# Kernel tuning notes

Measured on AMD Instinct MI355X. Metric: run time of the kernel, lower is better.

The kernel has to match this reference:

```python
import jax, jax.numpy as jnp
import numpy as np

B, C, H, W, RED = 32, 128, 32, 32, 8
CR = C // RED


def pw(w, x):
    # 1x1 conv as channel contraction: w [O,Cin], x [B,Cin,H,W]
    return jnp.einsum('oc,bchw->bohw', w, x)


def dw(x, k):
    # depthwise 3x3, SAME padding; k [C,1,3,3]
    return jax.lax.conv_general_dilated(
        x, k, (1, 1), 'SAME', feature_group_count=C,
        dimension_numbers=('NCHW', 'OIHW', 'NCHW'))


def setup_inputs() -> dict:
    key = jax.random.key(0)
    ks = jax.random.split(key, 32)
    s = 0.05
    d = {
        'h_t': jax.random.normal(ks[0], (B, C, H, W), jnp.float32),
        'm_prev': jax.random.normal(ks[1], (B, C, H, W), jnp.float32),
        'wq_h': jax.random.normal(ks[2], (CR, C)) * s,
        'wk_h': jax.random.normal(ks[3], (CR, C)) * s,
        'wv_h': jax.random.normal(ks[4], (C, C)) * s,
        'wk_m': jax.random.normal(ks[5], (CR, C)) * s,
        'wv_m': jax.random.normal(ks[6], (C, C)) * s,
        'wz_w': jax.random.normal(ks[7], (C, 2 * C)) * s,
        'wz_b': jnp.zeros((C,)),
        'wmi_dw': jax.random.normal(ks[8], (C, 1, 3, 3)) * s,
        'wmi_pw': jax.random.normal(ks[9], (C, C)) * s,
        'whi_dw': jax.random.normal(ks[10], (C, 1, 3, 3)) * s,
        'whi_pw': jax.random.normal(ks[11], (C, C)) * s,
        'bi': jnp.zeros((C,)),
        'wmg_dw': jax.random.normal(ks[12], (C, 1, 3, 3)) * s,
        'wmg_pw': jax.random.normal(ks[13], (C, C)) * s,
        'whg_dw': jax.random.normal(ks[14], (C, 1, 3, 3)) * s,
        'whg_pw': jax.random.normal(ks[15], (C, C)) * s,
        'bg': jnp.zeros((C,)),
        'wmo_dw': jax.random.normal(ks[16], (C, 1, 3, 3)) * s,
        'wmo_pw': jax.random.normal(ks[17], (C, C)) * s,
        'who_dw': jax.random.normal(ks[18], (C, 1, 3, 3)) * s,
        'who_pw': jax.random.normal(ks[19], (C, C)) * s,
        'bo': jnp.zeros((C,)),
        'wf_w': jax.random.normal(ks[20], (C, C)) * s,
        'wf_b': jnp.zeros((C,)),
    }
    return d


def reference(h_t, m_prev, wq_h, wk_h, wv_h, wk_m, wv_m, wz_w, wz_b,
              wmi_dw, wmi_pw, whi_dw, whi_pw, bi,
              wmg_dw, wmg_pw, whg_dw, whg_pw, bg,
              wmo_dw, wmo_pw, who_dw, who_pw, bo, wf_w, wf_b):
    b, c, h, w = h_t.shape
    N = h * w
    # shared-Q dual attention; Q/K are [B,Cr,N], V are [B,C,N]
    Q = pw(wq_h, h_t).reshape(b, -1, N)
    K_h = pw(wk_h, h_t).reshape(b, -1, N)
    V_h = pw(wv_h, h_t).reshape(b, c, N)
    attn_h = jax.nn.softmax(jnp.einsum('bki,bkj->bij', Q, K_h), axis=-1)  # [B,N,N]
    Z_h = jnp.einsum('bcj,bij->bci', V_h, attn_h).reshape(b, c, h, w)
    K_m = pw(wk_m, m_prev).reshape(b, -1, N)
    V_m = pw(wv_m, m_prev).reshape(b, c, N)
    attn_m = jax.nn.softmax(jnp.einsum('bki,bkj->bij', Q, K_m), axis=-1)
    Z_m = jnp.einsum('bcj,bij->bci', V_m, attn_m).reshape(b, c, h, w)
    Z = pw(wz_w, jnp.concatenate([Z_h, Z_m], axis=1)) + wz_b[None, :, None, None]
    # ConvLSTM-style gated fusion (depthwise 3x3 + pointwise 1x1 pairs)
    i_t = jax.nn.sigmoid(pw(wmi_pw, dw(Z, wmi_dw)) + pw(whi_pw, dw(h_t, whi_dw)) + bi[None, :, None, None])
    g_t = jnp.tanh(pw(wmg_pw, dw(Z, wmg_dw)) + pw(whg_pw, dw(h_t, whg_dw)) + bg[None, :, None, None])
    m_t = (1 - i_t) * m_prev + i_t * g_t
    o_t = jax.nn.sigmoid(pw(wmo_pw, dw(Z, wmo_dw)) + pw(who_pw, dw(h_t, who_dw)) + bo[None, :, None, None])
    h_out = o_t * m_t
    h_out = pw(wf_w, h_out) + wf_b[None, :, None, None] + h_t
    return (h_out, m_t)
```

## Files before the change

### kernel.cpp

```cpp
#include <hip/hip_runtime.h>
#include <hip/hip_bf16.h>
#include <math.h>

#define BB   32
#define CCH  128
#define NPIX 1024
#define CRED 16

typedef __attribute__((ext_vector_type(8)))  short short8;
typedef __attribute__((ext_vector_type(16))) float f32x16;

union Frag8 { short8 s8; unsigned u[4]; };

__device__ __forceinline__ unsigned pack2bf(float lo, float hi) {
    union { __hip_bfloat16 h; unsigned short u; } a, b;
    a.h = __float2bfloat16(lo);
    b.h = __float2bfloat16(hi);
    return (unsigned)a.u | ((unsigned)b.u << 16);
}

__global__ __launch_bounds__(256)
void wcvt_kernel(__hip_bfloat16* __restrict__ dst,
                 const float* __restrict__ s0, const float* __restrict__ s1,
                 const float* __restrict__ wz,
                 const float* __restrict__ s4, const float* __restrict__ s5,
                 const float* __restrict__ s6, const float* __restrict__ s7,
                 const float* __restrict__ s8, const float* __restrict__ s9,
                 const float* __restrict__ s10)
{
    const int slot = blockIdx.y;
    const int e = (blockIdx.x * 256 + threadIdx.x) * 4;
    const float* src;
    size_t soff;
    if (slot == 2 || slot == 3) {
        const int o = e >> 7, c = e & 127;
        src = wz;
        soff = (size_t)o * 256 + (slot == 3 ? 128 : 0) + c;
    } else {
        switch (slot) {
            case 0: src = s0; break;  case 1: src = s1; break;
            case 4: src = s4; break;  case 5: src = s5; break;
            case 6: src = s6; break;  case 7: src = s7; break;
            case 8: src = s8; break;  case 9: src = s9; break;
            default: src = s10; break;
        }
        soff = e;
    }
    float4 v = *(const float4*)&src[soff];
    uint2 pk = make_uint2(pack2bf(v.x, v.y), pack2bf(v.z, v.w));
    *(uint2*)&dst[(size_t)slot * 16384 + e] = pk;
}

__device__ __forceinline__ void stage_tile(char* buf, const float* Xb, int tid)
{
    const int p  = tid & 63;
    const int gb = tid >> 6;
    float xr[32];
    #pragma unroll
    for (int u = 0; u < 8; ++u) {
        const int c0 = (u * 4 + gb) * 4;
        #pragma unroll
        for (int j = 0; j < 4; ++j)
            xr[u * 4 + j] = Xb[(size_t)(c0 + j) * NPIX + p];
    }
    #pragma unroll
    for (int u = 0; u < 8; ++u) {
        const int g = u * 4 + gb;
        uint2 pk = make_uint2(pack2bf(xr[u * 4 + 0], xr[u * 4 + 1]),
                              pack2bf(xr[u * 4 + 2], xr[u * 4 + 3]));
        *(uint2*)(buf + p * 256 + ((g ^ (p & 31)) << 3)) = pk;
    }
}

__device__ __forceinline__ void stage_tile_bf16(char* buf,
                                                const __hip_bfloat16* Xb, int tid)
{
    const unsigned short* Xu = (const unsigned short*)Xb;
    const int p  = tid & 63;
    const int gb = tid >> 6;
    #pragma unroll
    for (int u = 0; u < 8; ++u) {
        const int g  = u * 4 + gb;
        const int c0 = g * 4;
        unsigned e0 = Xu[(size_t)(c0 + 0) * NPIX + p];
        unsigned e1 = Xu[(size_t)(c0 + 1) * NPIX + p];
        unsigned e2 = Xu[(size_t)(c0 + 2) * NPIX + p];
        unsigned e3 = Xu[(size_t)(c0 + 3) * NPIX + p];
        uint2 pk = make_uint2(e0 | (e1 << 16), e2 | (e3 << 16));
        *(uint2*)(buf + p * 256 + ((g ^ (p & 31)) << 3)) = pk;
    }
}

__device__ __forceinline__ void compute_pass(const char* buf,
                                             const __hip_bfloat16* W,
                                             f32x16* acc,
                                             int l31, int H, int ntw, int mth)
{
    const int prow = (32 * ntw + l31) * 256;
    #pragma unroll
    for (int kt = 0; kt < 8; ++kt) {
        Frag8 bf_;
        const int g0 = 4 * kt + 2 * H;
        *(uint2*)&bf_.u[0] = *(const uint2*)(buf + prow + (((g0    ) ^ l31) << 3));
        *(uint2*)&bf_.u[2] = *(const uint2*)(buf + prow + (((g0 + 1) ^ l31) << 3));
        #pragma unroll
        for (int mi = 0; mi < 2; ++mi) {
            const int m = 32 * (2 * mth + mi) + l31;
            short8 af = *(const short8*)&W[(size_t)m * 128 + 16 * kt + 8 * H];
            acc[mi] = __builtin_amdgcn_mfma_f32_32x32x16_bf16(af, bf_.s8, acc[mi], 0, 0, 0);
        }
    }
}

template<bool TWO, bool BF16IN, bool BF16OUT>
__global__ __launch_bounds__(256)
void pw_mfma(void* __restrict__ outv,
             const void* __restrict__ X1, const __hip_bfloat16* __restrict__ W1,
             const void* __restrict__ X2, const __hip_bfloat16* __restrict__ W2,
             const float* __restrict__ bias, const float* __restrict__ res)
{
    __shared__ __align__(16) char Xs[2][16384];
    const int tid = threadIdx.x;
    const int b   = blockIdx.y;
    const int p0  = blockIdx.x * 64;
    const int l31 = tid & 31;
    const int H   = (tid & 63) >> 5;
    const int w   = tid >> 6;
    const int ntw = w & 1;
    const int mth = w >> 1;
    const size_t boff = (size_t)b * CCH * NPIX + p0;

    if (BF16IN) stage_tile_bf16(&Xs[0][0], (const __hip_bfloat16*)X1 + boff, tid);
    else        stage_tile     (&Xs[0][0], (const float*)X1 + boff, tid);
    if (TWO) {
        if (BF16IN) stage_tile_bf16(&Xs[1][0], (const __hip_bfloat16*)X2 + boff, tid);
        else        stage_tile     (&Xs[1][0], (const float*)X2 + boff, tid);
    }
    __syncthreads();

    f32x16 acc[2];
    #pragma unroll
    for (int mi = 0; mi < 2; ++mi)
        #pragma unroll
        for (int e = 0; e < 16; ++e) acc[mi][e] = 0.f;

    compute_pass(&Xs[0][0], W1, acc, l31, H, ntw, mth);
    if (TWO)
        compute_pass(&Xs[1][0], W2, acc, l31, H, ntw, mth);

    const int pg = p0 + 32 * ntw + l31;
    #pragma unroll
    for (int mi = 0; mi < 2; ++mi) {
        const int mtile = 2 * mth + mi;
        #pragma unroll
        for (int r = 0; r < 16; ++r) {
            const int m = 32 * mtile + (r & 3) + 8 * (r >> 2) + 4 * H;
            float v = acc[mi][r];
            if (bias) v += bias[m];
            const size_t off = ((size_t)b * CCH + m) * NPIX + pg;
            if (res) v += res[off];
            if (BF16OUT) ((__hip_bfloat16*)outv)[off] = __float2bfloat16(v);
            else         ((float*)outv)[off] = v;
        }
    }
}

__global__ __launch_bounds__(256)
void qkproj_kernel(__hip_bfloat16* __restrict__ Qt,
                   __hip_bfloat16* __restrict__ Kht,
                   __hip_bfloat16* __restrict__ Kmt,
                   const float* __restrict__ h_t,
                   const float* __restrict__ m_prev,
                   const float* __restrict__ wq,
                   const float* __restrict__ wkh,
                   const float* __restrict__ wkm)
{
    const int b  = blockIdx.y;
    const int p0 = blockIdx.x * 128;
    const float* X; const float* W; __hip_bfloat16* Out;
    if (blockIdx.z == 0)      { X = h_t;    W = wq;  Out = Qt;  }
    else if (blockIdx.z == 1) { X = h_t;    W = wkh; Out = Kht; }
    else                      { X = m_prev; W = wkm; Out = Kmt; }

    __shared__ float Ws[16][128];
    __shared__ float Xs[32][132];
    const int tid = threadIdx.x;
    for (int i = tid; i < 16 * 128; i += 256)
        Ws[i / 128][i % 128] = W[i];

    const float* Xb = X + (size_t)b * CCH * NPIX;
    const int pl = tid & 127;
    const int h8 = tid >> 7;

    float acc[8];
    #pragma unroll
    for (int e = 0; e < 8; ++e) acc[e] = 0.f;

    for (int c0 = 0; c0 < CCH; c0 += 32) {
        __syncthreads();
        for (int idx = tid; idx < 32 * 32; idx += 256) {
            int r = idx >> 5, cp = (idx & 31) << 2;
            *(float4*)&Xs[r][cp] =
                *(const float4*)&Xb[(size_t)(c0 + r) * NPIX + p0 + cp];
        }
        __syncthreads();
        #pragma unroll 8
        for (int cc = 0; cc < 32; ++cc) {
            float xv = Xs[cc][pl];
            #pragma unroll
            for (int e = 0; e < 8; ++e)
                acc[e] += Ws[h8 * 8 + e][c0 + cc] * xv;
        }
    }

    Frag8 f;
    #pragma unroll
    for (int w = 0; w < 4; ++w)
        f.u[w] = pack2bf(acc[2 * w], acc[2 * w + 1]);
    *(short8*)&Out[((size_t)b * NPIX + p0 + pl) * 16 + 8 * h8] = f.s8;
}

__global__ __launch_bounds__(256)
void dw6_kernel(__hip_bfloat16* __restrict__ D, size_t SVe,
                const float* __restrict__ Z, const float* __restrict__ h_t,
                const float* __restrict__ wmi, const float* __restrict__ wmg,
                const float* __restrict__ wmo,
                const float* __restrict__ whi, const float* __restrict__ whg,
                const float* __restrict__ who)
{
    const int c = blockIdx.x, b = blockIdx.y;
    const float* src; const float *kaw, *kbw, *kcw;
    __hip_bfloat16* dbase;
    if (blockIdx.z == 0) { src = Z;   kaw = wmi; kbw = wmg; kcw = wmo; dbase = D; }
    else                 { src = h_t; kaw = whi; kbw = whg; kcw = who; dbase = D + 3 * SVe; }
    src += ((size_t)b * CCH + c) * NPIX;

    float ka[9], kb[9], kc[9];
    #pragma unroll
    for (int j = 0; j < 9; ++j) {
        ka[j] = kaw[c * 9 + j];
        kb[j] = kbw[c * 9 + j];
        kc[j] = kcw[c * 9 + j];
    }

    __shared__ float t[34][36];
    const int tid = threadIdx.x;
    for (int idx = tid; idx < 34 * 34; idx += 256) {
        int y = idx / 34, x = idx % 34;
        int gy = y - 1, gx = x - 1;
        t[y][x] = (gy >= 0 && gy < 32 && gx >= 0 && gx < 32)
                      ? src[gy * 32 + gx] : 0.f;
    }
    __syncthreads();
    const int x = tid % 32, y0 = tid / 32;
    #pragma unroll
    for (int q = 0; q < 4; ++q) {
        int y = y0 + 8 * q;
        float s0 = 0.f, s1 = 0.f, s2 = 0.f;
        #pragma unroll
        for (int dy = 0; dy < 3; ++dy)
            #pragma unroll
            for (int dx = 0; dx < 3; ++dx) {
                float tv = t[y + dy][x + dx];
                s0 += tv * ka[dy * 3 + dx];
                s1 += tv * kb[dy * 3 + dx];
                s2 += tv * kc[dy * 3 + dx];
            }
        const size_t o = ((size_t)(b * 32 + y) * CCH + c) * 32 + x;
        dbase[o]           = __float2bfloat16(s0);
        dbase[SVe + o]     = __float2bfloat16(s1);
        dbase[2 * SVe + o] = __float2bfloat16(s2);
    }
}

__device__ __forceinline__ void pass32(const char* buf,
                                       const __hip_bfloat16* W,
                                       f32x16* acc, int l31, int H, int wv)
{
    const int prow = l31 * 256;
    #pragma unroll
    for (int kt = 0; kt < 8; ++kt) {
        Frag8 bf_;
        const int g0 = 4 * kt + 2 * H;
        *(uint2*)&bf_.u[0] = *(const uint2*)(buf + prow + (((g0    ) ^ l31) << 3));
        *(uint2*)&bf_.u[2] = *(const uint2*)(buf + prow + (((g0 + 1) ^ l31) << 3));
        const int m = 32 * wv + l31;
        short8 af = *(const short8*)&W[(size_t)m * 128 + 16 * kt + 8 * H];
        *acc = __builtin_amdgcn_mfma_f32_32x32x16_bf16(af, bf_.s8, *acc, 0, 0, 0);
    }
}

__global__ __launch_bounds__(256)
void gates3_kernel(float* __restrict__ mt_out, float* __restrict__ hout,
                   const __hip_bfloat16* __restrict__ D, size_t SVe,
                   const __hip_bfloat16* __restrict__ Wg,
                   const __hip_bfloat16* __restrict__ Wf,
                   const float* __restrict__ bi, const float* __restrict__ bg,
                   const float* __restrict__ bo, const float* __restrict__ wfb,
                   const float* __restrict__ mp, const float* __restrict__ h_t)
{
    __shared__ __align__(16) char Xs[6][8192];
    const int tid = threadIdx.x;
    const int y   = blockIdx.x;
    const int b   = blockIdx.y;
    const int l31 = tid & 31;
    const int H   = (tid & 63) >> 5;
    const int wv  = tid >> 6;
    const size_t tbase = (size_t)(b * 32 + y) * 4096;

    const int cs = tid >> 1;
    const int ph = (tid & 1) << 4;
    const int gs = cs >> 2;
    const int cb = (cs & 3) << 1;
    #pragma unroll
    for (int s = 0; s < 6; ++s) {
        const unsigned short* src =
            (const unsigned short*)(D + (size_t)s * SVe + tbase + cs * 32 + ph);
        short8 va = *(const short8*)(src);
        short8 vb = *(const short8*)(src + 8);
        char* buf = &Xs[s][0];
        #pragma unroll
        for (int j = 0; j < 8; ++j) {
            const int pa = ph + j, pb2 = ph + 8 + j;
            *(unsigned short*)(buf + pa  * 256 + ((gs ^ pa)  << 3) + cb) =
                (unsigned short)va[j];
            *(unsigned short*)(buf + pb2 * 256 + ((gs ^ pb2) << 3) + cb) =
                (unsigned short)vb[j];
        }
    }

    const int pg = (y << 5) + l31;
    float mpv[16];
    #pragma unroll
    for (int r = 0; r < 16; ++r) {
        const int m = 32 * wv + (r & 3) + 8 * (r >> 2) + 4 * H;
        mpv[r] = mp[((size_t)b * CCH + m) * NPIX + pg];
    }

    __syncthreads();

    f32x16 aI, aG, aO;
    #pragma unroll
    for (int e = 0; e < 16; ++e) { aI[e] = 0.f; aG[e] = 0.f; aO[e] = 0.f; }

    pass32(&Xs[0][0], Wg + 0 * 16384, &aI, l31, H, wv);
    pass32(&Xs[3][0], Wg + 1 * 16384, &aI, l31, H, wv);
    pass32(&Xs[1][0], Wg + 2 * 16384, &aG, l31, H, wv);
    pass32(&Xs[4][0], Wg + 3 * 16384, &aG, l31, H, wv);
    pass32(&Xs[2][0], Wg + 4 * 16384, &aO, l31, H, wv);
    pass32(&Xs[5][0], Wg + 5 * 16384, &aO, l31, H, wv);

    float om[16];
    #pragma unroll
    for (int r = 0; r < 16; ++r) {
        const int m = 32 * wv + (r & 3) + 8 * (r >> 2) + 4 * H;
        const size_t off = ((size_t)b * CCH + m) * NPIX + pg;
        float it = 1.f / (1.f + __expf(-(aI[r] + bi[m])));
        float gt = tanhf(aG[r] + bg[m]);
        float ot = 1.f / (1.f + __expf(-(aO[r] + bo[m])));
        float mpv_r = mpv[r];
        float mt = (1.f - it) * mpv_r + it * gt;
        mt_out[off] = mt;
        om[r] = ot * mt;
    }

    __syncthreads();
    #pragma unroll
    for (int q = 0; q < 4; ++q) {
        const int g = 8 * wv + 2 * q + H;
        uint2 pk = make_uint2(pack2bf(om[4 * q + 0], om[4 * q + 1]),
                              pack2bf(om[4 * q + 2], om[4 * q + 3]));
        *(uint2*)(&Xs[0][0] + l31 * 256 + ((g ^ l31) << 3)) = pk;
    }
    __syncthreads();

    f32x16 aF;
    #pragma unroll
    for (int e = 0; e < 16; ++e) aF[e] = 0.f;
    pass32(&Xs[0][0], Wf, &aF, l31, H, wv);

    #pragma unroll
    for (int r = 0; r < 16; ++r) {
        const int m = 32 * wv + (r & 3) + 8 * (r >> 2) + 4 * H;
        const size_t off = ((size_t)b * CCH + m) * NPIX + pg;
        hout[off] = aF[r] + wfb[m] + h_t[off];
    }
}

__global__ __launch_bounds__(256)
void attn_mfma_kernel(__hip_bfloat16* __restrict__ Zh,
                      __hip_bfloat16* __restrict__ Zm,
                      const __hip_bfloat16* __restrict__ Qt,
                      const __hip_bfloat16* __restrict__ Kht,
                      const __hip_bfloat16* __restrict__ Kmt,
                      const __hip_bfloat16* __restrict__ Vh,
                      const __hip_bfloat16* __restrict__ Vm)
{
    const int b  = blockIdx.y;
    const int i0 = blockIdx.x * 128;
    const __hip_bfloat16* Kt; const __hip_bfloat16* Vg; __hip_bfloat16* Og;
    if (blockIdx.z == 0) { Kt = Kht; Vg = Vh; Og = Zh; }
    else                 { Kt = Kmt; Vg = Vm; Og = Zm; }
    Kt += (size_t)b * NPIX * 16;
    Vg += (size_t)b * CCH * NPIX;
    Og += (size_t)b * CCH * NPIX;

    __shared__ __align__(16) char Vs[2][128 * 64 * 2];

    const int tid = threadIdx.x;
    const int w   = tid >> 6;
    const int l   = tid & 63;
    const int l31 = l & 31;
    const int H   = l >> 5;

    const __hip_bfloat16* Qb = Qt + (size_t)b * NPIX * 16;
    short8 qf = *(const short8*)&Qb[((size_t)(i0 + 32 * w + l31)) * 16 + 8 * H];

    f32x16 acc[4];
    #pragma unroll
    for (int ct = 0; ct < 4; ++ct)
        #pragma unroll
        for (int e = 0; e < 16; ++e) acc[ct][e] = 0.f;
    float l_acc = 0.f;

    int cu[4], ldsoff[4]; size_t goff[4];
    #pragma unroll
    for (int u = 0; u < 4; ++u) {
        int idx = tid + 256 * u;
        cu[u] = idx >> 3;
        int jg = idx & 7;
        ldsoff[u] = cu[u] * 128 + ((jg ^ (cu[u] & 7)) << 4);
        goff[u]   = (size_t)cu[u] * NPIX + 8 * jg;
    }
    const int slotx_base = (l31 & 7);

    short8 v0 = *(const short8*)&Vg[goff[0]];
    short8 v1 = *(const short8*)&Vg[goff[1]];
    short8 v2 = *(const short8*)&Vg[goff[2]];
    short8 v3 = *(const short8*)&Vg[goff[3]];
    short8 kf0 = *(const short8*)&Kt[(size_t)(0 + l31) * 16 + 8 * H];
    short8 kf1 = *(const short8*)&Kt[(size_t)(32 + l31) * 16 + 8 * H];

    for (int t = 0; t < 16; ++t) {
        char* buf = &Vs[t & 1][0];
        *(short8*)(buf + ldsoff[0]) = v0;
        *(short8*)(buf + ldsoff[1]) = v1;
        *(short8*)(buf + ldsoff[2]) = v2;
        *(short8*)(buf + ldsoff[3]) = v3;

        short8 kn0 = kf0, kn1 = kf1;
        if (t < 15) {
            const int jn = (t + 1) * 64;
            v0 = *(const short8*)&Vg[goff[0] + jn];
            v1 = *(const short8*)&Vg[goff[1] + jn];
            v2 = *(const short8*)&Vg[goff[2] + jn];
            v3 = *(const short8*)&Vg[goff[3] + jn];
            kn0 = *(const short8*)&Kt[(size_t)(jn + l31) * 16 + 8 * H];
            kn1 = *(const short8*)&Kt[(size_t)(jn + 32 + l31) * 16 + 8 * H];
        }
        __syncthreads();

        #pragma unroll
        for (int jt = 0; jt < 2; ++jt) {
            short8 kcur = (jt == 0) ? kf0 : kf1;
            f32x16 z;
            #pragma unroll
            for (int e = 0; e < 16; ++e) z[e] = 0.f;
            f32x16 s = __builtin_amdgcn_mfma_f32_32x32x16_bf16(kcur, qf, z, 0, 0, 0);

            float p[16];
            float ls = 0.f;
            #pragma unroll
            for (int r = 0; r < 16; ++r) { p[r] = __expf(s[r]); ls += p[r]; }
            l_acc += ls + __shfl_xor(ls, 32);

            unsigned w0[4], w1[4], x0[4], x1[4];
            #pragma unroll
            for (int g = 0; g < 4; ++g) {
                w0[g] = pack2bf(p[4 * g + 0], p[4 * g + 1]);
                w1[g] = pack2bf(p[4 * g + 2], p[4 * g + 3]);
            }
            #pragma unroll
            for (int g = 0; g < 4; ++g) {
                x0[g] = __shfl_xor(w0[g], 32);
                x1[g] = __shfl_xor(w1[g], 32);
            }
            #pragma unroll
            for (int js = 0; js < 2; ++js) {
                const int gA = 2 * js, gB = 2 * js + 1;
                Frag8 pb;
                pb.u[0] = H ? x0[gB] : w0[gA];
                pb.u[1] = H ? x1[gB] : w1[gA];
                pb.u[2] = H ? w0[gB] : x0[gA];
                pb.u[3] = H ? w1[gB] : x1[gA];
                const int slot = 4 * jt + 2 * js + H;
                const int sx   = (slot ^ slotx_base) << 4;
                #pragma unroll
                for (int ct = 0; ct < 4; ++ct) {
                    short8 vf = *(short8*)(buf + (32 * ct + l31) * 128 + sx);
                    acc[ct] = __builtin_amdgcn_mfma_f32_32x32x16_bf16(
                        vf, pb.s8, acc[ct], 0, 0, 0);
                }
            }
        }
        kf0 = kn0; kf1 = kn1;
    }

    const float linv = 1.0f / l_acc;
    const int ig = i0 + 32 * w + l31;
    #pragma unroll
    for (int ct = 0; ct < 4; ++ct) {
        #pragma unroll
        for (int r = 0; r < 16; ++r) {
            int c = 32 * ct + (r & 3) + 8 * (r >> 2) + 4 * H;
            Og[(size_t)c * NPIX + ig] = __float2bfloat16(acc[ct][r] * linv);
        }
    }
}

extern "C" void kernel_launch(void* const* d_in, const int* in_sizes, int n_in,
                              void* d_out, int out_size, void* d_ws, size_t ws_size,
                              hipStream_t stream)
{
    (void)in_sizes; (void)n_in; (void)out_size; (void)ws_size;
    const float* h_t    = (const float*)d_in[0];
    const float* m_prev = (const float*)d_in[1];
    const float* wq_h   = (const float*)d_in[2];
    const float* wk_h   = (const float*)d_in[3];
    const float* wv_h   = (const float*)d_in[4];
    const float* wk_m   = (const float*)d_in[5];
    const float* wv_m   = (const float*)d_in[6];
    const float* wz_w   = (const float*)d_in[7];
    const float* wz_b   = (const float*)d_in[8];
    const float* wmi_dw = (const float*)d_in[9];
    const float* wmi_pw = (const float*)d_in[10];
    const float* whi_dw = (const float*)d_in[11];
    const float* whi_pw = (const float*)d_in[12];
    const float* bi     = (const float*)d_in[13];
    const float* wmg_dw = (const float*)d_in[14];
    const float* wmg_pw = (const float*)d_in[15];
    const float* whg_dw = (const float*)d_in[16];
    const float* whg_pw = (const float*)d_in[17];
    const float* bg     = (const float*)d_in[18];
    const float* wmo_dw = (const float*)d_in[19];
    const float* wmo_pw = (const float*)d_in[20];
    const float* who_dw = (const float*)d_in[21];
    const float* who_pw = (const float*)d_in[22];
    const float* bo     = (const float*)d_in[23];
    const float* wf_w   = (const float*)d_in[24];
    const float* wf_b   = (const float*)d_in[25];

    float* out = (float*)d_out;

    const size_t SQE = (size_t)BB * NPIX * CRED;
    const size_t SV  = (size_t)BB * CCH * NPIX;

    __hip_bfloat16* Wb  = (__hip_bfloat16*)d_ws;
    __hip_bfloat16* Qt  = Wb + 184320;
    __hip_bfloat16* Kht = Qt  + SQE;
    __hip_bfloat16* Kmt = Kht + SQE;
    __hip_bfloat16* Vhb = Kmt + SQE;
    __hip_bfloat16* Vmb = Vhb + SV;
    __hip_bfloat16* Zhb = Vmb + SV;
    __hip_bfloat16* Zmb = Zhb + SV;
    __hip_bfloat16* Dd  = Zmb + SV;
    float* Ev = (float*)(Dd + 6 * SV);

    dim3 blk(256);
    dim3 pwg(NPIX / 64, BB);

    wcvt_kernel<<<dim3(16, 11), blk, 0, stream>>>(
        Wb, wv_h, wv_m, wz_w, wmi_pw, whi_pw, wmg_pw, whg_pw, wmo_pw, who_pw, wf_w);

    qkproj_kernel<<<dim3(NPIX / 128, BB, 3), blk, 0, stream>>>(
        Qt, Kht, Kmt, h_t, m_prev, wq_h, wk_h, wk_m);
    pw_mfma<false, false, true><<<pwg, blk, 0, stream>>>(
        Vhb, h_t, Wb + 0 * 16384, nullptr, nullptr, nullptr, nullptr);
    pw_mfma<false, false, true><<<pwg, blk, 0, stream>>>(
        Vmb, m_prev, Wb + 1 * 16384, nullptr, nullptr, nullptr, nullptr);

    attn_mfma_kernel<<<dim3(NPIX / 128, BB, 2), blk, 0, stream>>>(
        Zhb, Zmb, Qt, Kht, Kmt, Vhb, Vmb);

    pw_mfma<true, true, false><<<pwg, blk, 0, stream>>>(
        Ev, Zhb, Wb + 2 * 16384, Zmb, Wb + 3 * 16384, wz_b, nullptr);

    dw6_kernel<<<dim3(CCH, BB, 2), blk, 0, stream>>>(
        Dd, SV, Ev, h_t, wmi_dw, wmg_dw, wmo_dw, whi_dw, whg_dw, who_dw);

    gates3_kernel<<<dim3(32, BB), blk, 0, stream>>>(
        out + SV, out, Dd, SV, Wb + 4 * 16384, Wb + 10 * 16384,
        bi, bg, bo, wf_b, m_prev, h_t);
}
```

Baseline: 288.5 us.

## Double-buffer gate tile staging in LDS and pipeline loads with MFMA passes

Replaces the upfront staging of all six depthwise-output tiles into 48KB of LDS with a two-buffer software pipeline. Register-held tiles are loaded from global memory one step ahead and scattered into alternating LDS buffers while MFMA passes run on the other buffer. It also changes the scatter to packed 8-byte stores, moves the m_prev load into the epilogue, and prefetches h_t before the final projection. LDS use drops, which could raise occupancy, at the cost of more barriers and exposed m_prev load latency.

```diff
diff --git a/kernel.cpp b/kernel.cpp
--- a/kernel.cpp
+++ b/kernel.cpp
@@ -273,6 +273,36 @@
     }
 }
 
+struct TileRegs { uint2 v[4]; };
+
+__device__ __forceinline__ void tload(TileRegs& t, const __hip_bfloat16* Dt,
+                                      int cq, int pq)
+{
+    const unsigned short* src = (const unsigned short*)Dt;
+    #pragma unroll
+    for (int j = 0; j < 4; ++j)
+        t.v[j] = *(const uint2*)(src + (4 * cq + j) * 32 + 4 * pq);
+}
+
+__device__ __forceinline__ unsigned half16(uint2 v, int i)
+{
+    unsigned w = (i < 2) ? v.x : v.y;
+    return (w >> ((i & 1) * 16)) & 0xFFFFu;
+}
+
+__device__ __forceinline__ void tscat(char* buf, const TileRegs& t,
+                                      int cq, int pq)
+{
+    #pragma unroll
+    for (int i = 0; i < 4; ++i) {
+        const int px = 4 * pq + i;
+        unsigned e0 = half16(t.v[0], i), e1 = half16(t.v[1], i);
+        unsigned e2 = half16(t.v[2], i), e3 = half16(t.v[3], i);
+        uint2 pk = make_uint2(e0 | (e1 << 16), e2 | (e3 << 16));
+        *(uint2*)(buf + px * 256 + ((cq ^ px) << 3)) = pk;
+    }
+}
+
 __device__ __forceinline__ void pass32(const char* buf,
                                        const __hip_bfloat16* W,
                                        f32x16* acc, int l31, int H, int wv)
@@ -299,57 +329,57 @@
                    const float* __restrict__ bo, const float* __restrict__ wfb,
                    const float* __restrict__ mp, const float* __restrict__ h_t)
 {
-    __shared__ __align__(16) char Xs[6][8192];
+    __shared__ __align__(16) char Xs0[8192];
+    __shared__ __align__(16) char Xs1[8192];
     const int tid = threadIdx.x;
     const int y   = blockIdx.x;
     const int b   = blockIdx.y;
     const int l31 = tid & 31;
     const int H   = (tid & 63) >> 5;
     const int wv  = tid >> 6;
+    const int cq  = tid >> 3;
+    const int pq  = tid & 7;
     const size_t tbase = (size_t)(b * 32 + y) * 4096;
 
-    const int cs = tid >> 1;
-    const int ph = (tid & 1) << 4;
-    const int gs = cs >> 2;
-    const int cb = (cs & 3) << 1;
-    #pragma unroll
-    for (int s = 0; s < 6; ++s) {
-        const unsigned short* src =
-            (const unsigned short*)(D + (size_t)s * SVe + tbase + cs * 32 + ph);
-        short8 va = *(const short8*)(src);
-        short8 vb = *(const short8*)(src + 8);
-        char* buf = &Xs[s][0];
-        #pragma unroll
-        for (int j = 0; j < 8; ++j) {
-            const int pa = ph + j, pb2 = ph + 8 + j;
-            *(unsigned short*)(buf + pa  * 256 + ((gs ^ pa)  << 3) + cb) =
-                (unsigned short)va[j];
-            *(unsigned short*)(buf + pb2 * 256 + ((gs ^ pb2) << 3) + cb) =
-                (unsigned short)vb[j];
-        }
-    }
+    const __hip_bfloat16* T0 = D + 0 * SVe + tbase;
+    const __hip_bfloat16* T1 = D + 3 * SVe + tbase;
+    const __hip_bfloat16* T2 = D + 1 * SVe + tbase;
+    const __hip_bfloat16* T3 = D + 4 * SVe + tbase;
+    const __hip_bfloat16* T4 = D + 2 * SVe + tbase;
+    const __hip_bfloat16* T5 = D + 5 * SVe + tbase;
+
+    f32x16 aI, aG, aO;
+    #pragma unroll
+    for (int e = 0; e < 16; ++e) { aI[e] = 0.f; aG[e] = 0.f; aO[e] = 0.f; }
+
+    TileRegs rva, rvb;
+    tload(rva, T0, cq, pq);
+    tload(rvb, T1, cq, pq);
+
+    tscat(Xs0, rva, cq, pq);
+    tload(rva, T2, cq, pq);
+    __syncthreads();
+    tscat(Xs1, rvb, cq, pq);
+    tload(rvb, T3, cq, pq);
+    pass32(Xs0, Wg + 0 * 16384, &aI, l31, H, wv);
+    __syncthreads();
+    tscat(Xs0, rva, cq, pq);
+    tload(rva, T4, cq, pq);
+    pass32(Xs1, Wg + 1 * 16384, &aI, l31, H, wv);
+    __syncthreads();
+    tscat(Xs1, rvb, cq, pq);
+    tload(rvb, T5, cq, pq);
+    pass32(Xs0, Wg + 2 * 16384, &aG, l31, H, wv);
+    __syncthreads();
+    tscat(Xs0, rva, cq, pq);
+    pass32(Xs1, Wg + 3 * 16384, &aG, l31, H, wv);
+    __syncthreads();
+    tscat(Xs1, rvb, cq, pq);
+    pass32(Xs0, Wg + 4 * 16384, &aO, l31, H, wv);
+    __syncthreads();
+    pass32(Xs1, Wg + 5 * 16384, &aO, l31, H, wv);
 
     const int pg = (y << 5) + l31;
-    float mpv[16];
-    #pragma unroll
-    for (int r = 0; r < 16; ++r) {
-        const int m = 32 * wv + (r & 3) + 8 * (r >> 2) + 4 * H;
-        mpv[r] = mp[((size_t)b * CCH + m) * NPIX + pg];
-    }
-
-    __syncthreads();
-
-    f32x16 aI, aG, aO;
-    #pragma unroll
-    for (int e = 0; e < 16; ++e) { aI[e] = 0.f; aG[e] = 0.f; aO[e] = 0.f; }
-
-    pass32(&Xs[0][0], Wg + 0 * 16384, &aI, l31, H, wv);
-    pass32(&Xs[3][0], Wg + 1 * 16384, &aI, l31, H, wv);
-    pass32(&Xs[1][0], Wg + 2 * 16384, &aG, l31, H, wv);
-    pass32(&Xs[4][0], Wg + 3 * 16384, &aG, l31, H, wv);
-    pass32(&Xs[2][0], Wg + 4 * 16384, &aO, l31, H, wv);
-    pass32(&Xs[5][0], Wg + 5 * 16384, &aO, l31, H, wv);
-
     float om[16];
     #pragma unroll
     for (int r = 0; r < 16; ++r) {
@@ -358,32 +388,37 @@
         float it = 1.f / (1.f + __expf(-(aI[r] + bi[m])));
         float gt = tanhf(aG[r] + bg[m]);
         float ot = 1.f / (1.f + __expf(-(aO[r] + bo[m])));
-        float mpv_r = mpv[r];
-        float mt = (1.f - it) * mpv_r + it * gt;
+        float mt = (1.f - it) * mp[off] + it * gt;
         mt_out[off] = mt;
         om[r] = ot * mt;
     }
 
-    __syncthreads();
+    float htv[16];
+    #pragma unroll
+    for (int r = 0; r < 16; ++r) {
+        const int m = 32 * wv + (r & 3) + 8 * (r >> 2) + 4 * H;
+        htv[r] = h_t[((size_t)b * CCH + m) * NPIX + pg];
+    }
+
     #pragma unroll
     for (int q = 0; q < 4; ++q) {
         const int g = 8 * wv + 2 * q + H;
         uint2 pk = make_uint2(pack2bf(om[4 * q + 0], om[4 * q + 1]),
                               pack2bf(om[4 * q + 2], om[4 * q + 3]));
-        *(uint2*)(&Xs[0][0] + l31 * 256 + ((g ^ l31) << 3)) = pk;
+        *(uint2*)(Xs0 + l31 * 256 + ((g ^ l31) << 3)) = pk;
     }
     __syncthreads();
 
     f32x16 aF;
     #pragma unroll
     for (int e = 0; e < 16; ++e) aF[e] = 0.f;
-    pass32(&Xs[0][0], Wf, &aF, l31, H, wv);
+    pass32(Xs0, Wf, &aF, l31, H, wv);
 
     #pragma unroll
     for (int r = 0; r < 16; ++r) {
         const int m = 32 * wv + (r & 3) + 8 * (r >> 2) + 4 * H;
         const size_t off = ((size_t)b * CCH + m) * NPIX + pg;
-        hout[off] = aF[r] + wfb[m] + h_t[off];
+        hout[off] = aF[r] + wfb[m] + htv[r];
     }
 }
 
```

New measurement: 281.6 us. -2.4%, faster.
